# Optimization experiments

Hardware: AMD Instinct MI355X
Metric: run time of the kernel (lower is better)

## Reference

```python
import jax, jax.numpy as jnp
import numpy as np

D = 128          # lattice edge (Z = Y = X = 128)
S = 8            # state_size
H = 16           # hidden_size
IN = 7 * S       # own state + 6 neighbor states = 56


def setup_inputs() -> dict:
    key = jax.random.key(0)
    k0, k1, k2 = jax.random.split(key, 3)
    N = D * D * D
    states = jax.random.normal(k0, (N, S), dtype=jnp.float32)
    W1 = jax.random.normal(k1, (IN, H), dtype=jnp.float32) * (1.0 / np.sqrt(IN))
    b1 = jnp.zeros((H,), dtype=jnp.float32)
    W2 = jax.random.normal(k2, (H, S), dtype=jnp.float32) * (1.0 / np.sqrt(H))
    b2 = jnp.zeros((S,), dtype=jnp.float32)
    return {"states": states, "W1": W1, "b1": b1, "W2": W2, "b2": b2}


def reference(states, W1, b1, W2, b2):
    # linear index = z*(X*Y) + y*X + x  ->  grid layout (Z, Y, X, S)
    g = states.reshape(D, D, D, S)
    # 6-neighbor gather with periodic boundary (NEIGHBOR_DIRECTIONS order:
    # (-1,0,0),(1,0,0),(0,-1,0),(0,1,0),(0,0,-1),(0,0,1)); x->axis2, y->axis1, z->axis0.
    # roll(+1) along an axis fetches the neighbor in the -1 direction.
    nbrs = [
        jnp.roll(g,  1, axis=2),  # x-1
        jnp.roll(g, -1, axis=2),  # x+1
        jnp.roll(g,  1, axis=1),  # y-1
        jnp.roll(g, -1, axis=1),  # y+1
        jnp.roll(g,  1, axis=0),  # z-1
        jnp.roll(g, -1, axis=0),  # z+1
    ]
    inp = jnp.concatenate([g] + nbrs, axis=-1)          # (Z, Y, X, 56)
    h = jnp.tanh(jnp.einsum('zyxi,ih->zyxh', inp, W1) + b1)
    out = jnp.einsum('zyxh,hs->zyxs', h, W2) + b2        # (Z, Y, X, 8)
    return out.reshape(-1, S)
```

## Files before the change

kernel.cpp:

```cpp
#include <hip/hip_runtime.h>

#define NTILE 131072

typedef __attribute__((ext_vector_type(8))) short bf16x8;
typedef __attribute__((ext_vector_type(4))) float f32x4;
typedef __attribute__((ext_vector_type(4))) unsigned int u32x4;

static __device__ __forceinline__ unsigned short f2bf_rne(float f) {
    union { float f; unsigned int i; } c; c.f = f;
    unsigned int u = c.i;
    return (unsigned short)((u + 0x7fffu + ((u >> 16) & 1u)) >> 16);
}
static __device__ __forceinline__ float bf2f(unsigned short u) {
    union { unsigned int i; float f; } c; c.i = ((unsigned int)u) << 16;
    return c.f;
}
static __device__ __forceinline__ unsigned int fbits(float f) {
    union { float f; unsigned int i; } c; c.f = f; return c.i;
}
static __device__ __forceinline__ unsigned int pack_bf16_rne(float lo, float hi) {
    unsigned int ul = fbits(lo), uh = fbits(hi);
    unsigned int tl = ul + 0x7fffu + ((ul >> 16) & 1u);
    unsigned int th = uh + 0x7fffu + ((uh >> 16) & 1u);
    return __builtin_amdgcn_perm(th, tl, 0x07060302u);
}

struct Frags {
    bf16x8 w1h0, w1l0, w1h1, w1l1, w2h, w2l;
    f32x4 b1v, b2v;
};

static __device__ __forceinline__ void build_frags(
    const float* W1, const float* b1, const float* W2, const float* b2,
    int col, int quad, Frags& F)
{
#pragma unroll
    for (int j = 0; j < 8; ++j) {
        int k0 = quad * 8 + j;
        float w = W1[k0 * 16 + col];
        unsigned short hi = f2bf_rne(w);
        F.w1h0[j] = (short)hi;
        F.w1l0[j] = (short)f2bf_rne(w - bf2f(hi));

        int k1 = 32 + quad * 8 + j;
        float wv = (k1 < 56) ? W1[k1 * 16 + col] : 0.0f;
        hi = f2bf_rne(wv);
        F.w1h1[j] = (short)hi;
        F.w1l1[j] = (short)f2bf_rne(wv - bf2f(hi));

        float w2 = (j < 4 && col < 8) ? W2[(quad * 4 + j) * 8 + col] : 0.0f;
        hi = f2bf_rne(w2);
        F.w2h[j] = (short)hi;
        F.w2l[j] = (short)f2bf_rne(w2 - bf2f(hi));
    }
#pragma unroll
    for (int r = 0; r < 4; ++r) {
        F.b1v[r] = b1[quad * 4 + r];
        F.b2v[r] = (quad < 2) ? b2[quad * 4 + r] : 0.0f;
    }
}

__global__ __launch_bounds__(64) void setup_kernel(
    const float* __restrict__ W1, const float* __restrict__ b1,
    const float* __restrict__ W2, const float* __restrict__ b2,
    u32x4* __restrict__ ws)
{
    const int lane = threadIdx.x;
    Frags F;
    build_frags(W1, b1, W2, b2, lane & 15, lane >> 4, F);
    union { bf16x8 v; u32x4 u; } c;
    c.v = F.w1h0; ws[0 * 64 + lane] = c.u;
    c.v = F.w1l0; ws[1 * 64 + lane] = c.u;
    c.v = F.w1h1; ws[2 * 64 + lane] = c.u;
    c.v = F.w1l1; ws[3 * 64 + lane] = c.u;
    c.v = F.w2h;  ws[4 * 64 + lane] = c.u;
    c.v = F.w2l;  ws[5 * 64 + lane] = c.u;
    union { f32x4 v; u32x4 u; } b;
    b.v = F.b1v; ws[6 * 64 + lane] = b.u;
    b.v = F.b2v; ws[7 * 64 + lane] = b.u;
}

template<bool USE_WS>
__global__ __launch_bounds__(256) void lattice_kernel(
    const float* __restrict__ states,
    const float* __restrict__ W1, const float* __restrict__ b1,
    const float* __restrict__ W2, const float* __restrict__ b2,
    float* __restrict__ out, const u32x4* __restrict__ ws)
{
    const int tid  = threadIdx.x;
    const int lane = tid & 63;
    const int wave = tid >> 6;
    const int col  = lane & 15;
    const int quad = lane >> 4;

    Frags F;
    if (USE_WS) {
        union { u32x4 u; bf16x8 v; } c;
        c.u = ws[0 * 64 + lane]; F.w1h0 = c.v;
        c.u = ws[1 * 64 + lane]; F.w1l0 = c.v;
        c.u = ws[2 * 64 + lane]; F.w1h1 = c.v;
        c.u = ws[3 * 64 + lane]; F.w1l1 = c.v;
        c.u = ws[4 * 64 + lane]; F.w2h  = c.v;
        c.u = ws[5 * 64 + lane]; F.w2l  = c.v;
        union { u32x4 u; f32x4 v; } b;
        b.u = ws[6 * 64 + lane]; F.b1v = b.v;
        b.u = ws[7 * 64 + lane]; F.b2v = b.v;
    } else {
        build_frags(W1, b1, W2, b2, col, quad, F);
    }

    const int dx0 = (quad == 1) ? -1 : (quad == 2) ? 1 : 0;
    const int dy0 = (quad == 3) ? -1 : 0;
    const int dy1 = (quad == 0 || quad == 3) ? 1 : 0;
    const int dz1 = (quad == 1) ? -1 : (quad == 2) ? 1 : 0;

    const int slab = blockIdx.x & 7;
    const int bq   = blockIdx.x >> 3;
    const int t0   = slab * 16384 + bq * 16 + wave * 4;

    f32x4 d0[4], d1[4], d2[4], d3[4];
#pragma unroll
    for (int j = 0; j < 4; ++j) {
        const int t = t0 + j;
        const int x = ((t & 7) << 4) + col;
        const int y = (t >> 3) & 127;
        const int z = t >> 10;
        const int x0 = (x + dx0) & 127;
        const int y0 = (y + dy0) & 127;
        const int n0 = (z << 14) | (y0 << 7) | x0;
        const int y1 = (y + dy1) & 127;
        const int z1 = (z + dz1) & 127;
        const int n1 = (z1 << 14) | (y1 << 7) | x;
        const float* p0 = states + (size_t)n0 * 8;
        const float* p1 = states + (size_t)n1 * 8;
        d0[j] = *(const f32x4*)p0;
        d1[j] = *(const f32x4*)(p0 + 4);
        d2[j] = *(const f32x4*)p1;
        d3[j] = *(const f32x4*)(p1 + 4);
    }

#pragma unroll
    for (int j = 0; j < 4; ++j) {
        union { bf16x8 v; unsigned int u[4]; } s0f, s1f;
        s0f.u[0] = __builtin_amdgcn_perm(fbits(d0[j][1]), fbits(d0[j][0]), 0x07060302u);
        s0f.u[1] = __builtin_amdgcn_perm(fbits(d0[j][3]), fbits(d0[j][2]), 0x07060302u);
        s0f.u[2] = __builtin_amdgcn_perm(fbits(d1[j][1]), fbits(d1[j][0]), 0x07060302u);
        s0f.u[3] = __builtin_amdgcn_perm(fbits(d1[j][3]), fbits(d1[j][2]), 0x07060302u);
        s1f.u[0] = __builtin_amdgcn_perm(fbits(d2[j][1]), fbits(d2[j][0]), 0x07060302u);
        s1f.u[1] = __builtin_amdgcn_perm(fbits(d2[j][3]), fbits(d2[j][2]), 0x07060302u);
        s1f.u[2] = __builtin_amdgcn_perm(fbits(d3[j][1]), fbits(d3[j][0]), 0x07060302u);
        s1f.u[3] = __builtin_amdgcn_perm(fbits(d3[j][3]), fbits(d3[j][2]), 0x07060302u);

        f32x4 acc = F.b1v;
        acc = __builtin_amdgcn_mfma_f32_16x16x32_bf16(F.w1h0, s0f.v, acc, 0, 0, 0);
        acc = __builtin_amdgcn_mfma_f32_16x16x32_bf16(F.w1l0, s0f.v, acc, 0, 0, 0);
        acc = __builtin_amdgcn_mfma_f32_16x16x32_bf16(F.w1h1, s1f.v, acc, 0, 0, 0);
        acc = __builtin_amdgcn_mfma_f32_16x16x32_bf16(F.w1l1, s1f.v, acc, 0, 0, 0);

        float h0t, h1t, h2t, h3t;
        {
            float e;
            e = __expf(2.0f * acc[0]); h0t = 1.0f - 2.0f * __builtin_amdgcn_rcpf(e + 1.0f);
            e = __expf(2.0f * acc[1]); h1t = 1.0f - 2.0f * __builtin_amdgcn_rcpf(e + 1.0f);
            e = __expf(2.0f * acc[2]); h2t = 1.0f - 2.0f * __builtin_amdgcn_rcpf(e + 1.0f);
            e = __expf(2.0f * acc[3]); h3t = 1.0f - 2.0f * __builtin_amdgcn_rcpf(e + 1.0f);
        }
        union { bf16x8 v; unsigned int u[4]; } hf;
        hf.u[0] = pack_bf16_rne(h0t, h1t);
        hf.u[1] = pack_bf16_rne(h2t, h3t);
        hf.u[2] = 0u;
        hf.u[3] = 0u;

        f32x4 acc2 = F.b2v;
        acc2 = __builtin_amdgcn_mfma_f32_16x16x32_bf16(F.w2h, hf.v, acc2, 0, 0, 0);
        acc2 = __builtin_amdgcn_mfma_f32_16x16x32_bf16(F.w2l, hf.v, acc2, 0, 0, 0);

        if (quad < 2) {
            *(f32x4*)(out + (size_t)((t0 + j) * 16 + col) * 8 + quad * 4) = acc2;
        }
    }
}

extern "C" void kernel_launch(void* const* d_in, const int* in_sizes, int n_in,
                              void* d_out, int out_size, void* d_ws, size_t ws_size,
                              hipStream_t stream) {
    const float* states = (const float*)d_in[0];
    const float* W1     = (const float*)d_in[1];
    const float* b1     = (const float*)d_in[2];
    const float* W2     = (const float*)d_in[3];
    const float* b2     = (const float*)d_in[4];
    float* out          = (float*)d_out;

    const bool use_ws = ws_size >= (size_t)(8 * 64 * 16);
    if (use_ws) {
        hipLaunchKernelGGL(setup_kernel, dim3(1), dim3(64), 0, stream,
                           W1, b1, W2, b2, (u32x4*)d_ws);
        hipLaunchKernelGGL((lattice_kernel<true>), dim3(8192), dim3(256), 0, stream,
                           states, W1, b1, W2, b2, out, (const u32x4*)d_ws);
    } else {
        hipLaunchKernelGGL((lattice_kernel<false>), dim3(8192), dim3(256), 0, stream,
                           states, W1, b1, W2, b2, out, (const u32x4*)d_ws);
    }
}
```

Before: 143.9 us.

## Stage neighbor rows in LDS per block for stencil reuse

Result: faster. 133.6 us (-7.1%).

```diff
diff --git a/kernel.cpp b/kernel.cpp
--- a/kernel.cpp
+++ b/kernel.cpp
@@ -1,6 +1,6 @@
 #include <hip/hip_runtime.h>
 
-#define NTILE 131072
+#define DIM 128
 
 typedef __attribute__((ext_vector_type(8))) short bf16x8;
 typedef __attribute__((ext_vector_type(4))) float f32x4;
@@ -81,12 +81,14 @@
 }
 
 template<bool USE_WS>
-__global__ __launch_bounds__(256) void lattice_kernel(
+__global__ __launch_bounds__(256, 2) void lattice_kernel(
     const float* __restrict__ states,
     const float* __restrict__ W1, const float* __restrict__ b1,
     const float* __restrict__ W2, const float* __restrict__ b2,
     float* __restrict__ out, const u32x4* __restrict__ ws)
 {
+    __shared__ __align__(16) float rows[14 * 1024];
+
     const int tid  = threadIdx.x;
     const int lane = tid & 63;
     const int wave = tid >> 6;
@@ -109,47 +111,60 @@
         build_frags(W1, b1, W2, b2, col, quad, F);
     }
 
-    const int dx0 = (quad == 1) ? -1 : (quad == 2) ? 1 : 0;
-    const int dy0 = (quad == 3) ? -1 : 0;
-    const int dy1 = (quad == 0 || quad == 3) ? 1 : 0;
-    const int dz1 = (quad == 1) ? -1 : (quad == 2) ? 1 : 0;
-
-    const int slab = blockIdx.x & 7;
-    const int bq   = blockIdx.x >> 3;
-    const int t0   = slab * 16384 + bq * 16 + wave * 4;
-
-    f32x4 d0[4], d1[4], d2[4], d3[4];
-#pragma unroll
-    for (int j = 0; j < 4; ++j) {
-        const int t = t0 + j;
-        const int x = ((t & 7) << 4) + col;
-        const int y = (t >> 3) & 127;
-        const int z = t >> 10;
-        const int x0 = (x + dx0) & 127;
-        const int y0 = (y + dy0) & 127;
-        const int n0 = (z << 14) | (y0 << 7) | x0;
-        const int y1 = (y + dy1) & 127;
-        const int z1 = (z + dz1) & 127;
-        const int n1 = (z1 << 14) | (y1 << 7) | x;
-        const float* p0 = states + (size_t)n0 * 8;
-        const float* p1 = states + (size_t)n1 * 8;
-        d0[j] = *(const f32x4*)p0;
-        d1[j] = *(const f32x4*)(p0 + 4);
-        d2[j] = *(const f32x4*)p1;
-        d3[j] = *(const f32x4*)(p1 + 4);
-    }
-
-#pragma unroll
-    for (int j = 0; j < 4; ++j) {
+    const int bI   = blockIdx.x;
+    const int slab = bI & 7;
+    const int inr  = bI >> 3;
+    const int z    = slab * 16 + (inr >> 5);
+    const int y0   = (inr & 31) << 2;
+
+    f32x4 tmp[14];
+#pragma unroll
+    for (int i = 0; i < 14; ++i) {
+        const int c  = wave * 14 + i;
+        const int r  = c >> 2;
+        const int p  = c & 3;
+        int yr, zr;
+        if (r < 6)       { yr = (y0 - 1 + r) & 127; zr = z; }
+        else if (r < 10) { yr = y0 + (r - 6);       zr = (z - 1) & 127; }
+        else             { yr = y0 + (r - 10);      zr = (z + 1) & 127; }
+        const float* g = states + (size_t)(zr * 16384 + yr * 128) * 8 + p * 256 + (lane << 2);
+        tmp[i] = *(const f32x4*)g;
+    }
+#pragma unroll
+    for (int i = 0; i < 14; ++i) {
+        const int c = wave * 14 + i;
+        const int r = c >> 2;
+        const int p = c & 3;
+        *(f32x4*)(&rows[r * 1024 + p * 256 + (lane << 2)]) = tmp[i];
+    }
+    __syncthreads();
+
+    const int rA  = (quad == 3) ? wave : wave + 1;
+    const int dxA = (quad == 1) ? -1 : (quad == 2) ? 1 : 0;
+    const int rB  = (quad == 1) ? 6 + wave : (quad == 2) ? 10 + wave : wave + 2;
+
+    const int outrow = z * 16384 + (y0 + wave) * 128;
+
+#pragma unroll
+    for (int i = 0; i < 8; ++i) {
+        const int X  = i << 4;
+        const int xA = (X + col + dxA) & 127;
+        const float* pA = &rows[rA * 1024 + xA * 8];
+        f32x4 a0 = *(const f32x4*)pA;
+        f32x4 a1 = *(const f32x4*)(pA + 4);
+        const float* pB = &rows[rB * 1024 + (X + col) * 8];
+        f32x4 c0 = *(const f32x4*)pB;
+        f32x4 c1 = *(const f32x4*)(pB + 4);
+
         union { bf16x8 v; unsigned int u[4]; } s0f, s1f;
-        s0f.u[0] = __builtin_amdgcn_perm(fbits(d0[j][1]), fbits(d0[j][0]), 0x07060302u);
-        s0f.u[1] = __builtin_amdgcn_perm(fbits(d0[j][3]), fbits(d0[j][2]), 0x07060302u);
-        s0f.u[2] = __builtin_amdgcn_perm(fbits(d1[j][1]), fbits(d1[j][0]), 0x07060302u);
-        s0f.u[3] = __builtin_amdgcn_perm(fbits(d1[j][3]), fbits(d1[j][2]), 0x07060302u);
-        s1f.u[0] = __builtin_amdgcn_perm(fbits(d2[j][1]), fbits(d2[j][0]), 0x07060302u);
-        s1f.u[1] = __builtin_amdgcn_perm(fbits(d2[j][3]), fbits(d2[j][2]), 0x07060302u);
-        s1f.u[2] = __builtin_amdgcn_perm(fbits(d3[j][1]), fbits(d3[j][0]), 0x07060302u);
-        s1f.u[3] = __builtin_amdgcn_perm(fbits(d3[j][3]), fbits(d3[j][2]), 0x07060302u);
+        s0f.u[0] = __builtin_amdgcn_perm(fbits(a0[1]), fbits(a0[0]), 0x07060302u);
+        s0f.u[1] = __builtin_amdgcn_perm(fbits(a0[3]), fbits(a0[2]), 0x07060302u);
+        s0f.u[2] = __builtin_amdgcn_perm(fbits(a1[1]), fbits(a1[0]), 0x07060302u);
+        s0f.u[3] = __builtin_amdgcn_perm(fbits(a1[3]), fbits(a1[2]), 0x07060302u);
+        s1f.u[0] = __builtin_amdgcn_perm(fbits(c0[1]), fbits(c0[0]), 0x07060302u);
+        s1f.u[1] = __builtin_amdgcn_perm(fbits(c0[3]), fbits(c0[2]), 0x07060302u);
+        s1f.u[2] = __builtin_amdgcn_perm(fbits(c1[1]), fbits(c1[0]), 0x07060302u);
+        s1f.u[3] = __builtin_amdgcn_perm(fbits(c1[3]), fbits(c1[2]), 0x07060302u);
 
         f32x4 acc = F.b1v;
         acc = __builtin_amdgcn_mfma_f32_16x16x32_bf16(F.w1h0, s0f.v, acc, 0, 0, 0);
@@ -176,7 +191,7 @@
         acc2 = __builtin_amdgcn_mfma_f32_16x16x32_bf16(F.w2l, hf.v, acc2, 0, 0, 0);
 
         if (quad < 2) {
-            *(f32x4*)(out + (size_t)((t0 + j) * 16 + col) * 8 + quad * 4) = acc2;
+            *(f32x4*)(out + (size_t)(outrow + X + col) * 8 + quad * 4) = acc2;
         }
     }
 }
@@ -195,10 +210,10 @@
     if (use_ws) {
         hipLaunchKernelGGL(setup_kernel, dim3(1), dim3(64), 0, stream,
                            W1, b1, W2, b2, (u32x4*)d_ws);
-        hipLaunchKernelGGL((lattice_kernel<true>), dim3(8192), dim3(256), 0, stream,
+        hipLaunchKernelGGL((lattice_kernel<true>), dim3(4096), dim3(256), 0, stream,
                            states, W1, b1, W2, b2, out, (const u32x4*)d_ws);
     } else {
-        hipLaunchKernelGGL((lattice_kernel<false>), dim3(8192), dim3(256), 0, stream,
+        hipLaunchKernelGGL((lattice_kernel<false>), dim3(4096), dim3(256), 0, stream,
                            states, W1, b1, W2, b2, out, (const u32x4*)d_ws);
     }
 }
```
